# Optimization experiments

Hardware: AMD Instinct MI355X
Metric: run time of the kernel (lower is better)

## Reference

```python
import jax, jax.numpy as jnp
import numpy as np

N = 100000  # nodes
E = 1600000  # edges (before self-loops)
F_IN, F_HID, F_OUT = 64, 128, 64


def setup_inputs() -> dict:
    key = jax.random.key(0)
    ks = jax.random.split(key, 8)
    x = jax.random.normal(ks[0], (N, F_IN), dtype=jnp.float32)
    edge_index = jax.random.randint(ks[1], (2, E), 0, N, dtype=jnp.int64)
    # Glorot-ish init for weights, zero bias (PyG GCNConv default)
    W1 = jax.random.normal(ks[2], (F_IN, F_HID), dtype=jnp.float32) / np.sqrt(F_IN)
    W2 = jax.random.normal(ks[3], (F_HID, F_HID), dtype=jnp.float32) / np.sqrt(F_HID)
    W3 = jax.random.normal(ks[4], (F_HID, F_OUT), dtype=jnp.float32) / np.sqrt(F_HID)
    b1 = jnp.zeros((F_HID,), dtype=jnp.float32)
    b2 = jnp.zeros((F_HID,), dtype=jnp.float32)
    b3 = jnp.zeros((F_OUT,), dtype=jnp.float32)
    return {"x": x, "edge_index": edge_index, "W1": W1, "b1": b1,
            "W2": W2, "b2": b2, "W3": W3, "b3": b3}


def _gcn_norm(edge_index, num_nodes):
    """Add self-loops and compute symmetric D^-1/2 A D^-1/2 edge norms."""
    loop = jnp.arange(num_nodes, dtype=edge_index.dtype)
    src = jnp.concatenate([edge_index[0], loop])  # [E+N]
    dst = jnp.concatenate([edge_index[1], loop])  # [E+N]
    deg = jax.ops.segment_sum(jnp.ones_like(src, dtype=jnp.float32), dst,
                              num_segments=num_nodes)
    dinv = jnp.where(deg > 0, jax.lax.rsqrt(deg), 0.0)
    norm = dinv[src] * dinv[dst]  # [E+N]
    return src, dst, norm


def _gcn_conv(h, src, dst, norm, W, b, num_nodes):
    hw = h @ W                                   # [N, out] dense transform
    msg = hw[src] * norm[:, None]                # gather + edge scale
    out = jax.ops.segment_sum(msg, dst, num_segments=num_nodes)  # scatter-add
    return out + b


def reference(x, edge_index, W1, b1, W2, b2, W3, b3):
    src, dst, norm = _gcn_norm(edge_index, N)
    h = jax.nn.relu(_gcn_conv(x, src, dst, norm, W1, b1, N))
    h = jax.nn.relu(_gcn_conv(h, src, dst, norm, W2, b2, N))
    return _gcn_conv(h, src, dst, norm, W3, b3, N)
```

## Files before the change

kernel.cpp:

```cpp
#include <hip/hip_runtime.h>
#include <hip/hip_bf16.h>
#include <hip/hip_fp16.h>


typedef _Float16 h8 __attribute__((ext_vector_type(8)));
typedef float f4 __attribute__((ext_vector_type(4)));

constexpr int BSHIFT = 7;
constexpr int BNODES = 1 << BSHIFT;
constexpr int PB     = 256;
constexpr int CAP    = 4096;

__device__ inline void load8h(const _Float16* p, float* f) {
    h8 v = *(const h8*)p;
#pragma unroll
    for (int j = 0; j < 8; j++) f[j] = (float)v[j];
}

__device__ inline void store8h(_Float16* p, const float* f) {
    h8 v;
#pragma unroll
    for (int j = 0; j < 8; j++) v[j] = (_Float16)f[j];
    *(h8*)p = v;
}

__device__ inline void store4h(_Float16* p, float4 v) {
    _Float16 t[4] = {(_Float16)v.x, (_Float16)v.y, (_Float16)v.z, (_Float16)v.w};
    *(uint2*)p = *(uint2*)t;
}

__global__ __launch_bounds__(256) void phist_k(const int* __restrict__ dst,
                                               int* __restrict__ hist,
                                               int* __restrict__ btot,
                                               int E, int nbuck, int chunk) {
    __shared__ int h[1024];
    for (int i = threadIdx.x; i < nbuck; i += 256) h[i] = 0;
    __syncthreads();
    int beg = blockIdx.x * chunk;
    int end = min(E, beg + chunk);
    for (int e = beg + threadIdx.x; e < end; e += 256)
        atomicAdd(&h[dst[e] >> BSHIFT], 1);
    __syncthreads();
    for (int i = threadIdx.x; i < nbuck; i += 256) {
        int v = h[i];
        hist[(long)blockIdx.x * nbuck + i] = v;
        if (v) atomicAdd(&btot[i], v);
    }
}

__global__ __launch_bounds__(256) void scan_blocks_k(const int* __restrict__ in,
                                                     int* __restrict__ excl,
                                                     int* __restrict__ bsums, int n) {
    __shared__ int s[256];
    int tid = threadIdx.x;
    int i = blockIdx.x * 256 + tid;
    int v = (i < n) ? in[i] : 0;
    s[tid] = v;
    __syncthreads();
    for (int off = 1; off < 256; off <<= 1) {
        int t = (tid >= off) ? s[tid - off] : 0;
        __syncthreads();
        s[tid] += t;
        __syncthreads();
    }
    if (i < n) excl[i] = s[tid] - v;
    if (tid == 255) bsums[blockIdx.x] = s[255];
}

__global__ __launch_bounds__(1024) void scan_sums_k(int* bsums, int nb) {
    __shared__ int s[1024];
    int tid = threadIdx.x;
    int v = (tid < nb) ? bsums[tid] : 0;
    s[tid] = v;
    __syncthreads();
    for (int off = 1; off < 1024; off <<= 1) {
        int t = (tid >= off) ? s[tid - off] : 0;
        __syncthreads();
        s[tid] += t;
        __syncthreads();
    }
    if (tid < nb) bsums[tid] = s[tid] - v;
}

__global__ __launch_bounds__(256) void finish_offs_k(int* __restrict__ offs,
                                                     const int* __restrict__ bsums,
                                                     int n) {
    int i = blockIdx.x * 256 + threadIdx.x;
    if (i < n) offs[i] += bsums[blockIdx.x];
}

__global__ __launch_bounds__(1024) void bbase_scan_k(const int* __restrict__ btot,
                                                     int* __restrict__ bbase,
                                                     int nbuck, int E) {
    __shared__ int s[1024];
    int tid = threadIdx.x;
    int v = (tid < nbuck) ? btot[tid] : 0;
    s[tid] = v;
    __syncthreads();
    for (int off = 1; off < 1024; off <<= 1) {
        int t = (tid >= off) ? s[tid - off] : 0;
        __syncthreads();
        s[tid] += t;
        __syncthreads();
    }
    if (tid < nbuck) bbase[tid] = s[tid] - v;
    if (tid == 0) bbase[nbuck] = E;
}

__global__ __launch_bounds__(256) void part2_k(const int* __restrict__ src,
                                               const int* __restrict__ dst,
                                               const int* __restrict__ offs,
                                               unsigned* __restrict__ ebuf,
                                               int E, int nbuck, int chunk) {
    __shared__ int cur[1024];
    for (int i = threadIdx.x; i < nbuck; i += 256)
        cur[i] = offs[(long)blockIdx.x * nbuck + i];
    __syncthreads();
    int beg = blockIdx.x * chunk;
    int end = min(E, beg + chunk);
    for (int e = beg + threadIdx.x; e < end; e += 256) {
        int d = dst[e];
        int b = d >> BSHIFT;
        int pos = atomicAdd(&cur[b], 1);
        ebuf[pos] = ((unsigned)(d & (BNODES - 1)) << 25) | (unsigned)src[e];
    }
}

__global__ __launch_bounds__(256) void finalize_k(const unsigned* __restrict__ ebuf,
                                                  const int* __restrict__ hist,
                                                  const int* __restrict__ offs,
                                                  const int* __restrict__ bbase,
                                                  int nbuck,
                                                  int* __restrict__ rowst,
                                                  int* __restrict__ rowend,
                                                  float* __restrict__ dinv,
                                                  int* __restrict__ col,
                                                  const float* __restrict__ x,
                                                  _Float16* __restrict__ msgX, int N) {
    __shared__ unsigned se[CAP];
    __shared__ int cj[PB], sj[PB], sb[PB];
    __shared__ int cnt_s[BNODES], scan_s[BNODES], cur_s[BNODES];
    __shared__ float di_s[BNODES];

    int b = blockIdx.x, tid = threadIdx.x;
    int node0 = b << BSHIFT;
    int nn = min(BNODES, N - node0);
    int beg = bbase[b];

    if (tid < PB) {
        cj[tid] = hist[(long)tid * nbuck + b];
        sj[tid] = offs[(long)tid * nbuck + b];
    }
    if (tid < BNODES) cnt_s[tid] = 0;
    __syncthreads();

    if (tid < PB) sb[tid] = cj[tid];
    __syncthreads();
    for (int off = 1; off < PB; off <<= 1) {
        int t = 0;
        if (tid < PB && tid >= off) t = sb[tid - off];
        __syncthreads();
        if (tid < PB) sb[tid] += t;
        __syncthreads();
    }
    int m = sb[PB - 1];
    __syncthreads();

    {
        int j = tid;
        int base = sb[j] - cj[j], c = cj[j], s0 = sj[j];
        for (int k = 0; k < c; k++) {
            unsigned e = ebuf[s0 + k];
            int idx = base + k;
            if (idx < CAP) se[idx] = e;
            else atomicAdd(&cnt_s[e >> 25], 1);
        }
    }
    __syncthreads();

    int mcap = m < CAP ? m : CAP;
    for (int i = tid; i < mcap; i += 256) atomicAdd(&cnt_s[se[i] >> 25], 1);
    __syncthreads();

    int v = (tid < BNODES) ? cnt_s[tid] : 0;
    if (tid < BNODES) scan_s[tid] = v;
    __syncthreads();
    for (int off = 1; off < BNODES; off <<= 1) {
        int t = 0;
        if (tid < BNODES && tid >= off) t = scan_s[tid - off];
        __syncthreads();
        if (tid < BNODES) scan_s[tid] += t;
        __syncthreads();
    }
    if (tid < nn) {
        int ex = scan_s[tid] - v;
        int st = beg + ex;
        rowst[node0 + tid] = st;
        rowend[node0 + tid] = st + v;
        float di = rsqrtf((float)v + 1.0f);
        dinv[node0 + tid] = di;
        di_s[tid] = di;
        cur_s[tid] = ex;
    }
    __syncthreads();

    for (int i = tid; i < mcap; i += 256) {
        unsigned e = se[i];
        int p = atomicAdd(&cur_s[e >> 25], 1);
        col[beg + p] = (int)(e & 0x1FFFFFFu);
    }
    if (m > CAP) {
        int j = tid;
        int base = sb[j] - cj[j], c = cj[j], s0 = sj[j];
        for (int k = 0; k < c; k++) {
            int idx = base + k;
            if (idx >= CAP) {
                unsigned e = ebuf[s0 + k];
                int p = atomicAdd(&cur_s[e >> 25], 1);
                col[beg + p] = (int)(e & 0x1FFFFFFu);
            }
        }
    }

    for (int t = tid; t < nn * 16; t += 256) {
        int nl = t >> 4, q = t & 15;
        int node = node0 + nl;
        float4 vx = *(const float4*)(x + (long)node * 64 + q * 4);
        float di = di_s[nl];
        vx.x *= di; vx.y *= di; vx.z *= di; vx.w *= di;
        store4h(msgX + (long)node * 64 + q * 4, vx);
    }
}

template <int F, bool BIAS, bool F16OUT>
__global__ __launch_bounds__(256) void agg_f16_k(const _Float16* __restrict__ msg,
                                                 const int* __restrict__ rowst,
                                                 const int* __restrict__ rowend,
                                                 const int* __restrict__ col,
                                                 const float* __restrict__ dinv,
                                                 const float* __restrict__ b,
                                                 void* __restrict__ out, int n) {
    constexpr int LPN = F / 8;
    constexpr int NPB = 256 / LPN;
    int node = blockIdx.x * NPB + threadIdx.x / LPN;
    int q = threadIdx.x % LPN;
    if (node >= n) return;

    float acc[8];
    load8h(msg + (long)node * F + q * 8, acc);

    int beg = rowst[node], end = rowend[node];
    int e = beg;
    for (; e + 4 <= end; e += 4) {
        int s0 = col[e], s1 = col[e + 1], s2 = col[e + 2], s3 = col[e + 3];
        float v0[8], v1[8], v2[8], v3[8];
        load8h(msg + (long)s0 * F + q * 8, v0);
        load8h(msg + (long)s1 * F + q * 8, v1);
        load8h(msg + (long)s2 * F + q * 8, v2);
        load8h(msg + (long)s3 * F + q * 8, v3);
#pragma unroll
        for (int j = 0; j < 8; j++) acc[j] += (v0[j] + v1[j]) + (v2[j] + v3[j]);
    }
    for (; e < end; e++) {
        int s = col[e];
        float v[8];
        load8h(msg + (long)s * F + q * 8, v);
#pragma unroll
        for (int j = 0; j < 8; j++) acc[j] += v[j];
    }

    float di = dinv[node];
    float o[8];
#pragma unroll
    for (int j = 0; j < 8; j++) o[j] = di * acc[j];
    if (BIAS) {
#pragma unroll
        for (int j = 0; j < 8; j++) o[j] += b[q * 8 + j];
    }
    if (F16OUT) {
        store8h((_Float16*)out + (long)node * F + q * 8, o);
    } else {
        float* dst = (float*)out + (long)node * F + q * 8;
        *(float4*)dst = make_float4(o[0], o[1], o[2], o[3]);
        *(float4*)(dst + 4) = make_float4(o[4], o[5], o[6], o[7]);
    }
}

template <int K, int FOUT>
__global__ __launch_bounds__(256) void wprep_k(const float* __restrict__ W,
                                               _Float16* __restrict__ Wsw) {
    constexpr int NT = FOUT / 16;
    int t = blockIdx.x * 256 + threadIdx.x;
    if (t >= (K / 32) * NT * 64) return;
    int lane = t & 63;
    int tile = (t >> 6) % NT;
    int chunk = (t >> 6) / NT;
    int kbase = chunk * 32 + (lane >> 4) * 8;
    int nc = tile * 16 + (lane & 15);
    h8 v;
#pragma unroll
    for (int j = 0; j < 8; j++) v[j] = (_Float16)W[(kbase + j) * FOUT + nc];
    ((h8*)Wsw)[t] = v;
}

template <int K, int FOUT, bool BIAS, bool RELU, bool DINV>
__global__ __launch_bounds__(256) void gemm_mfma_k(const _Float16* __restrict__ A,
                                                   const _Float16* __restrict__ Wsw,
                                                   const float* __restrict__ bias,
                                                   const float* __restrict__ dinv,
                                                   _Float16* __restrict__ C, int n) {
    constexpr int NT = FOUT / 16;
    constexpr int NC = K / 32;
    __shared__ _Float16 wl[K * FOUT];

    int tid = threadIdx.x;
    for (int i = tid; i < K * FOUT / 8; i += 256)
        ((h8*)wl)[i] = ((const h8*)Wsw)[i];
    __syncthreads();

    int lane = tid & 63, wave = tid >> 6;
    int quad = lane >> 4, cl = lane & 15;
    int row0 = blockIdx.x * 64 + wave * 16;

    h8 a[NC];
    const _Float16* arow = A + (long)(row0 + cl) * K + quad * 8;
#pragma unroll
    for (int c = 0; c < NC; c++) a[c] = *(const h8*)(arow + c * 32);

    f4 acc[NT];
#pragma unroll
    for (int t = 0; t < NT; t++) acc[t] = (f4){0.f, 0.f, 0.f, 0.f};

    const h8* wv = (const h8*)wl;
#pragma unroll
    for (int c = 0; c < NC; c++) {
#pragma unroll
        for (int t = 0; t < NT; t++)
            acc[t] = __builtin_amdgcn_mfma_f32_16x16x32_f16(
                a[c], wv[(c * NT + t) * 64 + lane], acc[t], 0, 0, 0);
    }

#pragma unroll
    for (int t = 0; t < NT; t++) {
        int c0 = t * 16 + cl;
        float bb = BIAS ? bias[c0] : 0.f;
#pragma unroll
        for (int r = 0; r < 4; r++) {
            int row = row0 + quad * 4 + r;
            if (row >= n) continue;
            float v = acc[t][r] + bb;
            if (RELU) v = fmaxf(v, 0.f);
            if (DINV) v *= dinv[row];
            C[(long)row * FOUT + c0] = (_Float16)v;
        }
    }
}

extern "C" void kernel_launch(void* const* d_in, const int* in_sizes, int n_in,
                              void* d_out, int out_size, void* d_ws, size_t ws_size,
                              hipStream_t stream) {
    const float* x  = (const float*)d_in[0];
    const int*   ei = (const int*)d_in[1];
    const float* W1 = (const float*)d_in[2];
    const float* b1 = (const float*)d_in[3];
    const float* W2 = (const float*)d_in[4];
    const float* b2 = (const float*)d_in[5];
    const float* W3 = (const float*)d_in[6];
    const float* b3 = (const float*)d_in[7];
    float* out = (float*)d_out;

    const int N = in_sizes[0] / 64;
    const int E = in_sizes[1] / 2;
    const int* src = ei;
    const int* dst = ei + E;
    const int nbuck = (N + BNODES - 1) >> BSHIFT;
    const int chunk = (E + PB - 1) / PB;
    const int n2 = PB * nbuck;
    const int nb2 = (n2 + 255) / 256;

    int*   hist   = (int*)d_ws;
    int*   offs   = hist + n2;
    int*   bsums  = offs + n2;
    int*   btot   = bsums + 1024;
    int*   bbase  = btot + nbuck;
    int*   rowst  = bbase + nbuck + 1;
    int*   rowend = rowst + N;
    float* dinv   = (float*)(rowend + N);
    int*   col    = (int*)(dinv + N);
    _Float16* w1s = (_Float16*)(col + E);
    _Float16* w2s = w1s + 64 * 128;
    _Float16* w3s = w2s + 128 * 128;
    float* P      = (float*)(w3s + 128 * 64);
    float* Q      = P + (long)N * 128;

    _Float16* msgX  = (_Float16*)P;
    unsigned* ebuf  = (unsigned*)Q;
    _Float16* aggX  = (_Float16*)Q;
    _Float16* msg1  = (_Float16*)P;
    _Float16* aggH1 = (_Float16*)Q;
    _Float16* h2    = (_Float16*)P;
    _Float16* msg3  = (_Float16*)Q;

    const int gb = (N + 63) / 64;

    wprep_k<64, 128><<<(64 * 128 / 8 + 255) / 256, 256, 0, stream>>>(W1, w1s);
    wprep_k<128, 128><<<(128 * 128 / 8 + 255) / 256, 256, 0, stream>>>(W2, w2s);
    wprep_k<128, 64><<<(128 * 64 / 8 + 255) / 256, 256, 0, stream>>>(W3, w3s);

    hipMemsetAsync(btot, 0, (size_t)nbuck * sizeof(int), stream);
    phist_k<<<PB, 256, 0, stream>>>(dst, hist, btot, E, nbuck, chunk);
    scan_blocks_k<<<nb2, 256, 0, stream>>>(hist, offs, bsums, n2);
    scan_sums_k<<<1, 1024, 0, stream>>>(bsums, nb2);
    finish_offs_k<<<nb2, 256, 0, stream>>>(offs, bsums, n2);
    bbase_scan_k<<<1, 1024, 0, stream>>>(btot, bbase, nbuck, E);
    part2_k<<<PB, 256, 0, stream>>>(src, dst, offs, ebuf, E, nbuck, chunk);
    finalize_k<<<nbuck, 256, 0, stream>>>(ebuf, hist, offs, bbase, nbuck,
                                          rowst, rowend, dinv, col, x, msgX, N);

    agg_f16_k<64, false, true><<<(N + 31) / 32, 256, 0, stream>>>(
        msgX, rowst, rowend, col, dinv, nullptr, (void*)aggX, N);
    gemm_mfma_k<64, 128, true, true, true><<<gb, 256, 0, stream>>>(
        aggX, w1s, b1, dinv, msg1, N);

    agg_f16_k<128, false, true><<<(N + 15) / 16, 256, 0, stream>>>(
        msg1, rowst, rowend, col, dinv, nullptr, (void*)aggH1, N);
    gemm_mfma_k<128, 128, true, true, false><<<gb, 256, 0, stream>>>(
        aggH1, w2s, b2, nullptr, h2, N);

    gemm_mfma_k<128, 64, false, false, true><<<gb, 256, 0, stream>>>(
        h2, w3s, nullptr, dinv, msg3, N);
    agg_f16_k<64, true, false><<<(N + 31) / 32, 256, 0, stream>>>(
        msg3, rowst, rowend, col, dinv, b3, (void*)out, N);
}
```

Measured before the change: 403.7 us.

## Fuse aggregation with MFMA GEMM and collapse preprocessing scan kernels

Adds a fused kernel that gathers neighbor rows into LDS for a 64-node tile, then runs the MFMA transform on that tile. This replaces separate aggregate and GEMM launches for layers 1 and 2 and removes the round trip of the aggregated intermediate through global memory. Preprocessing is also consolidated. Bucket totals are computed by column-summing the histogram in a merged scan kernel instead of with global atomics. The block-sum fixup is folded into consumers, and the three weight-prep kernels become one. The fused kernel has one gather per thread-row with less parallelism per node than the dedicated aggregation kernel and reads W fragments straight from global, which may hurt latency hiding.

```diff
diff --git a/kernel.cpp b/kernel.cpp
--- a/kernel.cpp
+++ b/kernel.cpp
@@ -31,7 +31,6 @@
 
 __global__ __launch_bounds__(256) void phist_k(const int* __restrict__ dst,
                                                int* __restrict__ hist,
-                                               int* __restrict__ btot,
                                                int E, int nbuck, int chunk) {
     __shared__ int h[1024];
     for (int i = threadIdx.x; i < nbuck; i += 256) h[i] = 0;
@@ -41,11 +40,8 @@
     for (int e = beg + threadIdx.x; e < end; e += 256)
         atomicAdd(&h[dst[e] >> BSHIFT], 1);
     __syncthreads();
-    for (int i = threadIdx.x; i < nbuck; i += 256) {
-        int v = h[i];
-        hist[(long)blockIdx.x * nbuck + i] = v;
-        if (v) atomicAdd(&btot[i], v);
-    }
+    for (int i = threadIdx.x; i < nbuck; i += 256)
+        hist[(long)blockIdx.x * nbuck + i] = h[i];
 }
 
 __global__ __launch_bounds__(256) void scan_blocks_k(const int* __restrict__ in,
@@ -67,10 +63,27 @@
     if (tid == 255) bsums[blockIdx.x] = s[255];
 }
 
-__global__ __launch_bounds__(1024) void scan_sums_k(int* bsums, int nb) {
+__global__ __launch_bounds__(1024) void mid_k(int* __restrict__ bsums, int nb,
+                                              const int* __restrict__ hist,
+                                              int* __restrict__ bbase,
+                                              int nbuck, int E) {
     __shared__ int s[1024];
     int tid = threadIdx.x;
-    int v = (tid < nb) ? bsums[tid] : 0;
+    int v = 0;
+    if (blockIdx.x == 0) {
+        v = (tid < nb) ? bsums[tid] : 0;
+    } else {
+        if (tid < nbuck) {
+            int t0 = 0, t1 = 0, t2 = 0, t3 = 0;
+            for (int j = 0; j < PB; j += 4) {
+                t0 += hist[(long)(j + 0) * nbuck + tid];
+                t1 += hist[(long)(j + 1) * nbuck + tid];
+                t2 += hist[(long)(j + 2) * nbuck + tid];
+                t3 += hist[(long)(j + 3) * nbuck + tid];
+            }
+            v = (t0 + t1) + (t2 + t3);
+        }
+    }
     s[tid] = v;
     __syncthreads();
     for (int off = 1; off < 1024; off <<= 1) {
@@ -79,42 +92,25 @@
         s[tid] += t;
         __syncthreads();
     }
-    if (tid < nb) bsums[tid] = s[tid] - v;
-}
-
-__global__ __launch_bounds__(256) void finish_offs_k(int* __restrict__ offs,
-                                                     const int* __restrict__ bsums,
-                                                     int n) {
-    int i = blockIdx.x * 256 + threadIdx.x;
-    if (i < n) offs[i] += bsums[blockIdx.x];
-}
-
-__global__ __launch_bounds__(1024) void bbase_scan_k(const int* __restrict__ btot,
-                                                     int* __restrict__ bbase,
-                                                     int nbuck, int E) {
-    __shared__ int s[1024];
-    int tid = threadIdx.x;
-    int v = (tid < nbuck) ? btot[tid] : 0;
-    s[tid] = v;
-    __syncthreads();
-    for (int off = 1; off < 1024; off <<= 1) {
-        int t = (tid >= off) ? s[tid - off] : 0;
-        __syncthreads();
-        s[tid] += t;
-        __syncthreads();
-    }
-    if (tid < nbuck) bbase[tid] = s[tid] - v;
-    if (tid == 0) bbase[nbuck] = E;
+    if (blockIdx.x == 0) {
+        if (tid < nb) bsums[tid] = s[tid] - v;
+    } else {
+        if (tid < nbuck) bbase[tid] = s[tid] - v;
+        if (tid == 0) bbase[nbuck] = E;
+    }
 }
 
 __global__ __launch_bounds__(256) void part2_k(const int* __restrict__ src,
                                                const int* __restrict__ dst,
                                                const int* __restrict__ offs,
+                                               const int* __restrict__ bsums,
                                                unsigned* __restrict__ ebuf,
                                                int E, int nbuck, int chunk) {
     __shared__ int cur[1024];
-    for (int i = threadIdx.x; i < nbuck; i += 256)
-        cur[i] = offs[(long)blockIdx.x * nbuck + i];
+    for (int i = threadIdx.x; i < nbuck; i += 256) {
+        long flat = (long)blockIdx.x * nbuck + i;
+        cur[i] = offs[flat] + bsums[flat >> 8];
+    }
     __syncthreads();
     int beg = blockIdx.x * chunk;
     int end = min(E, beg + chunk);
@@ -129,6 +125,7 @@
 __global__ __launch_bounds__(256) void finalize_k(const unsigned* __restrict__ ebuf,
                                                   const int* __restrict__ hist,
                                                   const int* __restrict__ offs,
+                                                  const int* __restrict__ bsums,
                                                   const int* __restrict__ bbase,
                                                   int nbuck,
                                                   int* __restrict__ rowst,
@@ -148,8 +145,9 @@
     int beg = bbase[b];
 
     if (tid < PB) {
-        cj[tid] = hist[(long)tid * nbuck + b];
-        sj[tid] = offs[(long)tid * nbuck + b];
+        long flat = (long)tid * nbuck + b;
+        cj[tid] = hist[flat];
+        sj[tid] = offs[flat] + bsums[flat >> 8];
     }
     if (tid < BNODES) cnt_s[tid] = 0;
     __syncthreads();
@@ -229,6 +227,103 @@
         float di = di_s[nl];
         vx.x *= di; vx.y *= di; vx.z *= di; vx.w *= di;
         store4h(msgX + (long)node * 64 + q * 4, vx);
+    }
+}
+
+template <int K, int FOUT, bool BIAS, bool RELU, bool DINV_OUT>
+__global__ __launch_bounds__(256) void fag_k(const _Float16* __restrict__ msg,
+                                             const int* __restrict__ rowst,
+                                             const int* __restrict__ rowend,
+                                             const int* __restrict__ col,
+                                             const float* __restrict__ dinv,
+                                             const _Float16* __restrict__ Wsw,
+                                             const float* __restrict__ bias,
+                                             _Float16* __restrict__ C, int n) {
+    constexpr int NT = FOUT / 16, NC = K / 32;
+    constexpr int LDK = K + 8;
+    __shared__ _Float16 As[64 * LDK];
+
+    int tid = threadIdx.x;
+    int row0 = blockIdx.x * 64;
+
+    constexpr int LPN = K / 8;
+    constexpr int NPB = 256 / LPN;
+#pragma unroll
+    for (int pass = 0; pass < 64 / NPB; pass++) {
+        int nl = pass * NPB + tid / LPN;
+        int q = tid % LPN;
+        int node = row0 + nl;
+        float acc[8];
+        if (node < n) {
+            load8h(msg + (long)node * K + q * 8, acc);
+            int beg = rowst[node], end = rowend[node];
+            int e = beg;
+            for (; e + 4 <= end; e += 4) {
+                int s0 = col[e], s1 = col[e + 1], s2 = col[e + 2], s3 = col[e + 3];
+                float v0[8], v1[8], v2[8], v3[8];
+                load8h(msg + (long)s0 * K + q * 8, v0);
+                load8h(msg + (long)s1 * K + q * 8, v1);
+                load8h(msg + (long)s2 * K + q * 8, v2);
+                load8h(msg + (long)s3 * K + q * 8, v3);
+#pragma unroll
+                for (int j = 0; j < 8; j++) acc[j] += (v0[j] + v1[j]) + (v2[j] + v3[j]);
+            }
+            for (; e < end; e++) {
+                int s = col[e];
+                float v[8];
+                load8h(msg + (long)s * K + q * 8, v);
+#pragma unroll
+                for (int j = 0; j < 8; j++) acc[j] += v[j];
+            }
+            float di = dinv[node];
+#pragma unroll
+            for (int j = 0; j < 8; j++) acc[j] *= di;
+        } else {
+#pragma unroll
+            for (int j = 0; j < 8; j++) acc[j] = 0.f;
+        }
+        h8 o;
+#pragma unroll
+        for (int j = 0; j < 8; j++) o[j] = (_Float16)acc[j];
+        *(h8*)(As + nl * LDK + q * 8) = o;
+    }
+    __syncthreads();
+
+    int lane = tid & 63, wave = tid >> 6;
+    int quad = lane >> 4, cl = lane & 15;
+    int r0 = wave * 16;
+
+    h8 a[NC];
+#pragma unroll
+    for (int c = 0; c < NC; c++)
+        a[c] = *(const h8*)(As + (r0 + cl) * LDK + quad * 8 + c * 32);
+
+    f4 acc2[NT];
+#pragma unroll
+    for (int t = 0; t < NT; t++) acc2[t] = (f4){0.f, 0.f, 0.f, 0.f};
+
+    const h8* wv = (const h8*)Wsw;
+#pragma unroll
+    for (int c = 0; c < NC; c++) {
+#pragma unroll
+        for (int t = 0; t < NT; t++)
+            acc2[t] = __builtin_amdgcn_mfma_f32_16x16x32_f16(
+                a[c], wv[(c * NT + t) * 64 + lane], acc2[t], 0, 0, 0);
+    }
+
+#pragma unroll
+    for (int t = 0; t < NT; t++) {
+        int c0 = t * 16 + cl;
+        float bb = BIAS ? bias[c0] : 0.f;
+#pragma unroll
+        for (int r = 0; r < 4; r++) {
+            int row = row0 + r0 + quad * 4 + r;
+            if (row >= n) continue;
+            float v = acc2[t][r] + bb;
+            if (RELU) v = fmaxf(v, 0.f);
+            if (DINV_OUT) v *= dinv[row];
+            C[(long)row * FOUT + c0] = (_Float16)v;
+        }
     }
 }
 
@@ -287,11 +382,9 @@
 }
 
 template <int K, int FOUT>
-__global__ __launch_bounds__(256) void wprep_k(const float* __restrict__ W,
-                                               _Float16* __restrict__ Wsw) {
+__device__ inline void wfrag(const float* __restrict__ W,
+                             _Float16* __restrict__ Wsw, int t) {
     constexpr int NT = FOUT / 16;
-    int t = blockIdx.x * 256 + threadIdx.x;
-    if (t >= (K / 32) * NT * 64) return;
     int lane = t & 63;
     int tile = (t >> 6) % NT;
     int chunk = (t >> 6) / NT;
@@ -301,6 +394,18 @@
 #pragma unroll
     for (int j = 0; j < 8; j++) v[j] = (_Float16)W[(kbase + j) * FOUT + nc];
     ((h8*)Wsw)[t] = v;
+}
+
+__global__ __launch_bounds__(256) void wprep3_k(const float* __restrict__ W1,
+                                                const float* __restrict__ W2,
+                                                const float* __restrict__ W3,
+                                                _Float16* __restrict__ w1s,
+                                                _Float16* __restrict__ w2s,
+                                                _Float16* __restrict__ w3s) {
+    int t = blockIdx.x * 256 + threadIdx.x;
+    if (t < 1024) wfrag<64, 128>(W1, w1s, t);
+    else if (t < 3072) wfrag<128, 128>(W2, w2s, t - 1024);
+    else if (t < 4096) wfrag<128, 64>(W3, w3s, t - 3072);
 }
 
 template <int K, int FOUT, bool BIAS, bool RELU, bool DINV>
@@ -381,8 +486,7 @@
     int*   hist   = (int*)d_ws;
     int*   offs   = hist + n2;
     int*   bsums  = offs + n2;
-    int*   btot   = bsums + 1024;
-    int*   bbase  = btot + nbuck;
+    int*   bbase  = bsums + 1024;
     int*   rowst  = bbase + nbuck + 1;
     int*   rowend = rowst + N;
     float* dinv   = (float*)(rowend + N);
@@ -393,39 +497,28 @@
     float* P      = (float*)(w3s + 128 * 64);
     float* Q      = P + (long)N * 128;
 
-    _Float16* msgX  = (_Float16*)P;
-    unsigned* ebuf  = (unsigned*)Q;
-    _Float16* aggX  = (_Float16*)Q;
-    _Float16* msg1  = (_Float16*)P;
-    _Float16* aggH1 = (_Float16*)Q;
-    _Float16* h2    = (_Float16*)P;
-    _Float16* msg3  = (_Float16*)Q;
+    _Float16* msgX = (_Float16*)P;
+    unsigned* ebuf = (unsigned*)Q;
+    _Float16* msg1 = (_Float16*)Q;
+    _Float16* h2   = (_Float16*)P;
+    _Float16* msg3 = (_Float16*)Q;
 
     const int gb = (N + 63) / 64;
 
-    wprep_k<64, 128><<<(64 * 128 / 8 + 255) / 256, 256, 0, stream>>>(W1, w1s);
-    wprep_k<128, 128><<<(128 * 128 / 8 + 255) / 256, 256, 0, stream>>>(W2, w2s);
-    wprep_k<128, 64><<<(128 * 64 / 8 + 255) / 256, 256, 0, stream>>>(W3, w3s);
-
-    hipMemsetAsync(btot, 0, (size_t)nbuck * sizeof(int), stream);
-    phist_k<<<PB, 256, 0, stream>>>(dst, hist, btot, E, nbuck, chunk);
+    wprep3_k<<<16, 256, 0, stream>>>(W1, W2, W3, w1s, w2s, w3s);
+
+    phist_k<<<PB, 256, 0, stream>>>(dst, hist, E, nbuck, chunk);
     scan_blocks_k<<<nb2, 256, 0, stream>>>(hist, offs, bsums, n2);
-    scan_sums_k<<<1, 1024, 0, stream>>>(bsums, nb2);
-    finish_offs_k<<<nb2, 256, 0, stream>>>(offs, bsums, n2);
-    bbase_scan_k<<<1, 1024, 0, stream>>>(btot, bbase, nbuck, E);
-    part2_k<<<PB, 256, 0, stream>>>(src, dst, offs, ebuf, E, nbuck, chunk);
-    finalize_k<<<nbuck, 256, 0, stream>>>(ebuf, hist, offs, bbase, nbuck,
+    mid_k<<<2, 1024, 0, stream>>>(bsums, nb2, hist, bbase, nbuck, E);
+    part2_k<<<PB, 256, 0, stream>>>(src, dst, offs, bsums, ebuf, E, nbuck, chunk);
+    finalize_k<<<nbuck, 256, 0, stream>>>(ebuf, hist, offs, bsums, bbase, nbuck,
                                           rowst, rowend, dinv, col, x, msgX, N);
 
-    agg_f16_k<64, false, true><<<(N + 31) / 32, 256, 0, stream>>>(
-        msgX, rowst, rowend, col, dinv, nullptr, (void*)aggX, N);
-    gemm_mfma_k<64, 128, true, true, true><<<gb, 256, 0, stream>>>(
-        aggX, w1s, b1, dinv, msg1, N);
-
-    agg_f16_k<128, false, true><<<(N + 15) / 16, 256, 0, stream>>>(
-        msg1, rowst, rowend, col, dinv, nullptr, (void*)aggH1, N);
-    gemm_mfma_k<128, 128, true, true, false><<<gb, 256, 0, stream>>>(
-        aggH1, w2s, b2, nullptr, h2, N);
+    fag_k<64, 128, true, true, true><<<gb, 256, 0, stream>>>(
+        msgX, rowst, rowend, col, dinv, w1s, b1, msg1, N);
+
+    fag_k<128, 128, true, true, false><<<gb, 256, 0, stream>>>(
+        msg1, rowst, rowend, col, dinv, w2s, b2, h2, N);
 
     gemm_mfma_k<128, 64, false, false, true><<<gb, 256, 0, stream>>>(
         h2, w3s, nullptr, dinv, msg3, N);
```

After: 391.3 us. 3.1% less time.
